# Performance work log

Hardware: AMD Instinct MI355X
Metric: run time of the kernel (lower is better)

Reference implementation:

```python
import jax, jax.numpy as jnp
import numpy as np

MODEL_DIM = 256
NUM_HEAD = 8
HEAD_DIM = MODEL_DIM // NUM_HEAD  # 32
ROT_DIM_AXIS = int(0.5 * HEAD_DIM)  # 16 per axis, 32 total rotated channels
LN_EPS = 1e-5
MASK_BIAS = -1e9  # fp32 precision
SCALE = HEAD_DIM ** -0.5
INIT_RANGE = 0.02
N_LAYERS = 6


def _rotate_half(x):
    # interleaved pairs: (d r) with r=2 -> (-x2, x1) re-interleaved
    x = x.reshape(*x.shape[:-1], -1, 2)
    x1, x2 = x[..., 0], x[..., 1]
    return jnp.stack([-x2, x1], axis=-1).reshape(*x.shape[:-2], -1)


def _axial_freqs(seqlen):
    # RotaryEmbedding('lang' freqs) over t = linspace(-1, 1, seqlen)
    inv_freq = 1.0 / (10000.0 ** (jnp.arange(0, ROT_DIM_AXIS, 2, dtype=jnp.float32) / ROT_DIM_AXIS))
    t = jnp.linspace(-1.0, 1.0, seqlen, dtype=jnp.float32)
    f = jnp.repeat(t[:, None] * inv_freq[None, :], 2, axis=-1)  # (s, ROT_DIM_AXIS)
    fh = jnp.broadcast_to(f[:, None, :], (seqlen, seqlen, ROT_DIM_AXIS))
    fw = jnp.broadcast_to(f[None, :, :], (seqlen, seqlen, ROT_DIM_AXIS))
    return jnp.concatenate([fh, fw], axis=-1)  # (s, s, 2*ROT_DIM_AXIS)


def _apply_rotary(freqs, t):
    rot_dim = freqs.shape[-1]
    t_rot, t_pass = t[..., :rot_dim], t[..., rot_dim:]
    t_rot = t_rot * jnp.cos(freqs) + _rotate_half(t_rot) * jnp.sin(freqs)
    return jnp.concatenate([t_rot, t_pass], axis=-1)


def setup_inputs() -> dict:
    key = jax.random.key(0)
    k1, k2, k3, k4 = jax.random.split(key, 4)
    b, s = 2, 128
    pair_act = jax.random.normal(k1, (b, s, s, MODEL_DIM), dtype=jnp.float32)
    pair_mask = jax.random.randint(k2, (b, s, s), 0, 2).astype(bool)  # True = masked
    Wqkv = jax.random.normal(k3, (3 * MODEL_DIM, MODEL_DIM), dtype=jnp.float32) * INIT_RANGE
    Wout = jax.random.normal(k4, (MODEL_DIM, MODEL_DIM), dtype=jnp.float32) * (INIT_RANGE / np.sqrt(2 * N_LAYERS))
    ln_gamma = jnp.ones((MODEL_DIM,), dtype=jnp.float32)
    ln_beta = jnp.zeros((MODEL_DIM,), dtype=jnp.float32)
    return {"pair_act": pair_act, "pair_mask": pair_mask, "ln_gamma": ln_gamma,
            "ln_beta": ln_beta, "Wqkv": Wqkv, "Wout": Wout}


def reference(pair_act, pair_mask, ln_gamma, ln_beta, Wqkv, Wout):
    # orientation == 'per_row': no axis swap
    b, s = pair_act.shape[0], pair_act.shape[1]
    # LayerNorm over model_dim
    mu = jnp.mean(pair_act, axis=-1, keepdims=True)
    var = jnp.var(pair_act, axis=-1, keepdims=True)
    x = (pair_act - mu) * jax.lax.rsqrt(var + LN_EPS) * ln_gamma + ln_beta
    # QKV projection (no bias)
    qkv = jnp.einsum('bxyd,ed->bxye', x, Wqkv)  # (b, s, s, 3*MODEL_DIM)
    q, k, v = jnp.split(qkv, 3, axis=-1)
    # 2D axial rotary on first 2*ROT_DIM_AXIS channels of the feature dim
    freqs = _axial_freqs(s)  # (s, s, 32)
    q = _apply_rotary(freqs, q)
    k = _apply_rotary(freqs, k)
    # multihead attention per row (axis s1 independent)
    q = q.reshape(b, s, s, NUM_HEAD, HEAD_DIM)
    k = k.reshape(b, s, s, NUM_HEAD, HEAD_DIM)
    v = v.reshape(b, s, s, NUM_HEAD, HEAD_DIM)
    scores = jnp.einsum('bxqhd,bxkhd->bxhqk', q, k) * SCALE  # (b, s1, h, s2, s2)
    mask = pair_mask[:, :, None, None, :]  # (b, s1, 1, 1, s2)
    scores = jnp.where(mask, MASK_BIAS, scores)
    attn = jax.nn.softmax(scores, axis=-1)
    out = jnp.einsum('bxhqk,bxkhd->bxqhd', attn, v).reshape(b, s, s, MODEL_DIM)
    return jnp.einsum('bxyd,ed->bxye', out, Wout)
```

## Files before the change

kernel.cpp:

```cpp
#include <hip/hip_runtime.h>
#include <math.h>
#include <stdint.h>

typedef __attribute__((ext_vector_type(8))) short short8;
typedef __attribute__((ext_vector_type(4))) float floatx4;

#define LN_EPS 1e-5f
#define ATT_SCALE 0.17677669529663687f

__device__ __constant__ float INVF[8] = {
    1.0f, 0.31622776601683794f, 0.1f, 0.031622776601683794f,
    0.01f, 0.0031622776601683794f, 0.001f, 0.00031622776601683794f};

__device__ inline unsigned short f2bf(float f) {
    unsigned u = __float_as_uint(f);
    u += 0x7fffu + ((u >> 16) & 1u);
    return (unsigned short)(u >> 16);
}

__device__ inline void gl_lds16(const unsigned short* g, unsigned short* l) {
    __builtin_amdgcn_global_load_lds(
        (const __attribute__((address_space(1))) void*)(uintptr_t)g,
        (__attribute__((address_space(3))) void*)(uintptr_t)l, 16, 0, 0);
}

__device__ inline void stage_tile(const unsigned short* __restrict__ Wsrc,
                                  unsigned short* dst, int w, int lane) {
    #pragma unroll
    for (int i = 0; i < 4; ++i) {
        int rbase = i * 16 + w * 2;
        int row = rbase + (lane >> 5);
        int sl = lane & 31;
        int c = (sl & ~7) | ((sl & 7) ^ (row & 7));
        gl_lds16(Wsrc + (size_t)row * 256 + c * 8, dst + rbase * 256);
    }
}

#define VM0() asm volatile("s_waitcnt vmcnt(0)" ::: "memory")
#define LG0() asm volatile("s_waitcnt lgkmcnt(0)" ::: "memory")
#define SBAR()                                 \
    do {                                       \
        __builtin_amdgcn_s_barrier();          \
        __builtin_amdgcn_sched_barrier(0);     \
    } while (0)

__global__ __launch_bounds__(256)
void prep_w(const float* __restrict__ wq, const float* __restrict__ wo,
            unsigned short* __restrict__ bq, unsigned short* __restrict__ bo) {
    int g = blockIdx.x * 256 + threadIdx.x;
    const float* src;
    unsigned short* dst;
    if (g < 49152) { src = wq + (size_t)g * 4; dst = bq + (size_t)g * 4; }
    else { int h = g - 49152; src = wo + (size_t)h * 4; dst = bo + (size_t)h * 4; }
    float4 v = *(const float4*)src;
    uint2 o;
    o.x = (unsigned)f2bf(v.x) | ((unsigned)f2bf(v.y) << 16);
    o.y = (unsigned)f2bf(v.z) | ((unsigned)f2bf(v.w) << 16);
    *(uint2*)dst = o;
}

__global__ __launch_bounds__(512, 2)
void fused_kernel(const float* __restrict__ pair_act, const int* __restrict__ mask,
                  const float* __restrict__ gamma, const float* __restrict__ beta,
                  const unsigned short* __restrict__ Wqkv,
                  const unsigned short* __restrict__ Wout,
                  float* __restrict__ out) {
    __shared__ __align__(16) unsigned short S16[2][16384];
    __shared__ __align__(16) unsigned short Ks[2][128 * 40];
    __shared__ __align__(16) unsigned short Vt[2][32 * 136];
    __shared__ __align__(16) unsigned short Qall[8 * 640];

    int bx = blockIdx.x;
    int tid = threadIdx.x;
    int w = tid >> 6, lane = tid & 63, qd = lane >> 4, lo = lane & 15;
    unsigned short* Qscr = Qall + w * 640;

    float tX = -1.0f + (2.0f / 127.0f) * (float)(bx & 127);

    stage_tile(Wqkv, &S16[1][0], w, lane);

    float msel[8];
    #pragma unroll
    for (int nt = 0; nt < 8; ++nt)
        msel[nt] = mask[bx * 128 + nt * 16 + lo] ? 0.0f : 1.0f;

    short8 a_frag[8];
    {
        int rl = tid >> 2, q0 = tid & 3;
        const float* src = pair_act + ((size_t)(bx * 128 + rl)) * 256 + q0 * 4;
        float4 v[16];
        float s = 0.f;
        #pragma unroll
        for (int u = 0; u < 16; ++u) {
            v[u] = *(const float4*)(src + u * 16);
            s += v[u].x + v[u].y + v[u].z + v[u].w;
        }
        s += __shfl_xor(s, 1);
        s += __shfl_xor(s, 2);
        float mean = s * (1.0f / 256.0f);
        float sq = 0.f;
        #pragma unroll
        for (int u = 0; u < 16; ++u) {
            float d0 = v[u].x - mean, d1 = v[u].y - mean;
            float d2 = v[u].z - mean, d3 = v[u].w - mean;
            sq += d0 * d0 + d1 * d1 + d2 * d2 + d3 * d3;
        }
        sq += __shfl_xor(sq, 1);
        sq += __shfl_xor(sq, 2);
        float rs = rsqrtf(sq * (1.0f / 256.0f) + LN_EPS);

        int rw = 16 * w + lo;
        #pragma unroll
        for (int p = 0; p < 2; ++p) {
            #pragma unroll
            for (int ul = 0; ul < 8; ++ul) {
                int u = p * 8 + ul;
                float4 g4 = *(const float4*)(gamma + q0 * 4 + u * 16);
                float4 b4 = *(const float4*)(beta + q0 * 4 + u * 16);
                unsigned e0 = f2bf((v[u].x - mean) * rs * g4.x + b4.x);
                unsigned e1 = f2bf((v[u].y - mean) * rs * g4.y + b4.y);
                unsigned e2 = f2bf((v[u].z - mean) * rs * g4.z + b4.z);
                unsigned e3 = f2bf((v[u].w - mean) * rs * g4.w + b4.w);
                int cw = 2 * ul + (q0 >> 1);
                int ss = (cw & ~7) | ((cw & 7) ^ (rl & 7));
                uint2 pk;
                pk.x = e0 | (e1 << 16);
                pk.y = e2 | (e3 << 16);
                *(uint2*)&S16[0][rl * 128 + ss * 8 + (q0 & 1) * 4] = pk;
            }
            __syncthreads();
            #pragma unroll
            for (int cp = 0; cp < 4; ++cp) {
                int ci = cp * 4 + qd;
                int ss = (ci & ~7) | ((ci & 7) ^ (rw & 7));
                a_frag[p * 4 + cp] = *(const short8*)&S16[0][rw * 128 + ss * 8];
            }
            __syncthreads();
        }
    }

    unsigned q_pk[4][4][2], k_pk[4][4][2], v_pk[4][4][2];
    #pragma unroll
    for (int t = 0; t < 12; ++t) {
        VM0();
        SBAR();
        const unsigned short* nsrc =
            (t < 11) ? (Wqkv + (size_t)(t + 1) * 64 * 256) : Wout;
        stage_tile(nsrc, &S16[t & 1][0], w, lane);

        const unsigned short* Sb = &S16[(t + 1) & 1][0];
        floatx4 acc[4];
        #pragma unroll
        for (int tq = 0; tq < 4; ++tq) acc[tq] = (floatx4){0.f, 0.f, 0.f, 0.f};
        #pragma unroll
        for (int cc = 0; cc < 8; ++cc) {
            #pragma unroll
            for (int tq = 0; tq < 4; ++tq) {
                int rw2 = tq * 16 + lo;
                int ci = cc * 4 + qd;
                int ss = (ci & ~7) | ((ci & 7) ^ (rw2 & 7));
                short8 bf = *(const short8*)&Sb[rw2 * 256 + ss * 8];
                acc[tq] = __builtin_amdgcn_mfma_f32_16x16x32_bf16(
                    a_frag[cc], bf, acc[tq], 0, 0, 0);
            }
        }
        if (t == 0 || t == 4) {
            #pragma unroll
            for (int tc = 0; tc < 2; ++tc) {
                int pi = (tc * 16 + lo) >> 1;
                float invf = INVF[pi & 7];
                float sgn = (lo & 1) ? 1.0f : -1.0f;
                #pragma unroll
                for (int r = 0; r < 4; ++r) {
                    int y = 16 * w + qd * 4 + r;
                    float tp = (pi < 8) ? tX
                                        : (-1.0f + (2.0f / 127.0f) * (float)y);
                    float sn, cs;
                    __sincosf(tp * invf, &sn, &cs);
                    float vv = acc[tc][r];
                    float pv = __shfl_xor(vv, 1);
                    acc[tc][r] = vv * cs + sgn * pv * sn;
                }
            }
        }
        int part = t >> 2, hc = t & 3;
        #pragma unroll
        for (int tq = 0; tq < 4; ++tq) {
            unsigned p0 = (unsigned)f2bf(acc[tq][0]) |
                          ((unsigned)f2bf(acc[tq][1]) << 16);
            unsigned p1 = (unsigned)f2bf(acc[tq][2]) |
                          ((unsigned)f2bf(acc[tq][3]) << 16);
            if (part == 0) { q_pk[hc][tq][0] = p0; q_pk[hc][tq][1] = p1; }
            else if (part == 1) { k_pk[hc][tq][0] = p0; k_pk[hc][tq][1] = p1; }
            else { v_pk[hc][tq][0] = p0; v_pk[hc][tq][1] = p1; }
        }
    }

    {
        #pragma unroll
        for (int tt = 0; tt < 2; ++tt) {
            int tC = tt;
            int d = tt * 16 + lo;
            #pragma unroll
            for (int r = 0; r < 4; ++r) {
                unsigned kv = (k_pk[0][tC][r >> 1] >> ((r & 1) * 16)) & 0xffffu;
                Ks[0][(16 * w + qd * 4 + r) * 40 + d] = (unsigned short)kv;
            }
            uint2 pv;
            pv.x = v_pk[0][tC][0];
            pv.y = v_pk[0][tC][1];
            *(uint2*)&Vt[0][d * 136 + 16 * w + qd * 4] = pv;
        }
    }
    LG0();
    SBAR();
    stage_tile(Wout + (size_t)64 * 256, &S16[0][0], w, lane);

    short8 of[8];
    #pragma unroll
    for (int h = 0; h < 8; ++h) {
        if (h < 7) {
            int g = h + 1, hcg = g >> 1, tg0 = (g & 1) * 2, kb = g & 1;
            #pragma unroll
            for (int tt = 0; tt < 2; ++tt) {
                int tC = tg0 + tt;
                int d = tt * 16 + lo;
                #pragma unroll
                for (int r = 0; r < 4; ++r) {
                    unsigned kv =
                        (k_pk[hcg][tC][r >> 1] >> ((r & 1) * 16)) & 0xffffu;
                    Ks[kb][(16 * w + qd * 4 + r) * 40 + d] = (unsigned short)kv;
                }
                uint2 pv;
                pv.x = v_pk[hcg][tC][0];
                pv.y = v_pk[hcg][tC][1];
                *(uint2*)&Vt[kb][d * 136 + 16 * w + qd * 4] = pv;
            }
        }
        {
            int hch = h >> 1, cb = h & 1;
            #pragma unroll
            for (int tt = 0; tt < 2; ++tt) {
                int tC = (h & 1) * 2 + tt;
                #pragma unroll
                for (int r = 0; r < 4; ++r) {
                    unsigned qv =
                        (q_pk[hch][tC][r >> 1] >> ((r & 1) * 16)) & 0xffffu;
                    Qscr[(qd * 4 + r) * 40 + tt * 16 + lo] = (unsigned short)qv;
                }
            }
            short8 aq = *(const short8*)&Qscr[lo * 40 + qd * 8];
            float ef[8][4];
            float sums[4] = {0.f, 0.f, 0.f, 0.f};
            #pragma unroll
            for (int nt = 0; nt < 8; ++nt) {
                short8 bk = *(const short8*)&Ks[cb][(nt * 16 + lo) * 40 + qd * 8];
                floatx4 c = (floatx4){0.f, 0.f, 0.f, 0.f};
                c = __builtin_amdgcn_mfma_f32_16x16x32_bf16(aq, bk, c, 0, 0, 0);
                #pragma unroll
                for (int r = 0; r < 4; ++r) {
                    float e = __expf(c[r] * ATT_SCALE) * msel[nt];
                    ef[nt][r] = e;
                    sums[r] += e;
                }
            }
            float inv[4];
            #pragma unroll
            for (int r = 0; r < 4; ++r) {
                float vv = sums[r];
                vv += __shfl_xor(vv, 1);
                vv += __shfl_xor(vv, 2);
                vv += __shfl_xor(vv, 4);
                vv += __shfl_xor(vv, 8);
                inv[r] = 1.0f / vv;
            }
            floatx4 o2[2];
            o2[0] = (floatx4){0.f, 0.f, 0.f, 0.f};
            o2[1] = (floatx4){0.f, 0.f, 0.f, 0.f};
            #pragma unroll
            for (int c2 = 0; c2 < 4; ++c2) {
                #pragma unroll
                for (int half = 0; half < 2; ++half) {
                    int nt = c2 * 2 + half;
                    #pragma unroll
                    for (int r = 0; r < 4; ++r)
                        Qscr[(qd * 4 + r) * 40 + half * 16 + lo] =
                            f2bf(ef[nt][r]);
                }
                short8 pa = *(const short8*)&Qscr[lo * 40 + qd * 8];
                #pragma unroll
                for (int n = 0; n < 2; ++n) {
                    short8 vb = *(const short8*)&Vt[cb][(n * 16 + lo) * 136 +
                                                       c2 * 32 + qd * 8];
                    o2[n] = __builtin_amdgcn_mfma_f32_16x16x32_bf16(pa, vb,
                                                                    o2[n], 0, 0, 0);
                }
            }
            #pragma unroll
            for (int n = 0; n < 2; ++n)
                #pragma unroll
                for (int r = 0; r < 4; ++r)
                    Qscr[(qd * 4 + r) * 40 + n * 16 + lo] =
                        f2bf(o2[n][r] * inv[r]);
            of[h] = *(const short8*)&Qscr[lo * 40 + qd * 8];
        }
        LG0();
        if (h == 7) VM0();
        SBAR();
    }

    #pragma unroll
    for (int nc = 0; nc < 4; ++nc) {
        if (nc) {
            VM0();
            SBAR();
            if (nc < 3)
                stage_tile(Wout + (size_t)(nc + 1) * 64 * 256,
                           &S16[nc & 1][0], w, lane);
        }
        const unsigned short* Sb = &S16[(nc + 1) & 1][0];
        floatx4 acc[4];
        #pragma unroll
        for (int tq = 0; tq < 4; ++tq) acc[tq] = (floatx4){0.f, 0.f, 0.f, 0.f};
        #pragma unroll
        for (int cc = 0; cc < 8; ++cc) {
            #pragma unroll
            for (int tq = 0; tq < 4; ++tq) {
                int rw2 = tq * 16 + lo;
                int ci = cc * 4 + qd;
                int ss = (ci & ~7) | ((ci & 7) ^ (rw2 & 7));
                short8 bf = *(const short8*)&Sb[rw2 * 256 + ss * 8];
                acc[tq] = __builtin_amdgcn_mfma_f32_16x16x32_bf16(
                    of[cc], bf, acc[tq], 0, 0, 0);
            }
        }
        #pragma unroll
        for (int tq = 0; tq < 4; ++tq)
            #pragma unroll
            for (int r = 0; r < 4; ++r)
                out[(size_t)(bx * 128 + 16 * w + qd * 4 + r) * 256 + nc * 64 +
                    tq * 16 + lo] = acc[tq][r];
    }
}

extern "C" void kernel_launch(void* const* d_in, const int* in_sizes, int n_in,
                              void* d_out, int out_size, void* d_ws, size_t ws_size,
                              hipStream_t stream) {
    const float* pair_act = (const float*)d_in[0];
    const int* pair_mask = (const int*)d_in[1];
    const float* ln_gamma = (const float*)d_in[2];
    const float* ln_beta = (const float*)d_in[3];
    const float* Wqkv = (const float*)d_in[4];
    const float* Wout = (const float*)d_in[5];
    float* out = (float*)d_out;

    char* ws = (char*)d_ws;
    unsigned short* wqkv_bf = (unsigned short*)ws;
    unsigned short* wout_bf = (unsigned short*)(ws + 393216);

    prep_w<<<256, 256, 0, stream>>>(Wqkv, Wout, wqkv_bf, wout_bf);
    fused_kernel<<<256, 512, 0, stream>>>(pair_act, pair_mask, ln_gamma, ln_beta,
                                          wqkv_bf, wout_bf, out);
}
```

Before: 138.3 us.

## Compute transposed scores and route P to MFMA A-operand via lane shuffles

The attention inner loop now computes S^T (K as A operand, Q as B) so each lane holds scores per key, then packs exp values to bf16 and redistributes them with ds_bpermute shuffles into the A-operand layout for the PV MFMA, instead of staging P through LDS scratch. Score, exp and PV MMA are interleaved per 32-key chunk, and the row sum is reduced with two shuffles. The Q fragment for the next head is prefetched into a double-buffered scratch region, doubling per-wave Q scratch LDS. This removes LDS round trips and register pressure from holding all exp values, at the cost of many cross-lane shuffles and extra mask broadcasts.

```diff
diff --git a/kernel.cpp b/kernel.cpp
--- a/kernel.cpp
+++ b/kernel.cpp
@@ -68,12 +68,12 @@
     __shared__ __align__(16) unsigned short S16[2][16384];
     __shared__ __align__(16) unsigned short Ks[2][128 * 40];
     __shared__ __align__(16) unsigned short Vt[2][32 * 136];
-    __shared__ __align__(16) unsigned short Qall[8 * 640];
+    __shared__ __align__(16) unsigned short Qall[8 * 1280];
 
     int bx = blockIdx.x;
     int tid = threadIdx.x;
     int w = tid >> 6, lane = tid & 63, qd = lane >> 4, lo = lane & 15;
-    unsigned short* Qscr = Qall + w * 640;
+    unsigned short* Qscr = Qall + w * 1280;
 
     float tX = -1.0f + (2.0f / 127.0f) * (float)(bx & 127);
 
@@ -196,6 +196,13 @@
         }
     }
 
+    float m2[8][4];
+    #pragma unroll
+    for (int nt = 0; nt < 8; ++nt)
+        #pragma unroll
+        for (int r = 0; r < 4; ++r)
+            m2[nt][r] = __shfl(msel[nt], qd * 4 + r);
+
     {
         #pragma unroll
         for (int tt = 0; tt < 2; ++tt) {
@@ -216,6 +223,14 @@
     SBAR();
     stage_tile(Wout + (size_t)64 * 256, &S16[0][0], w, lane);
 
+    #pragma unroll
+    for (int tt = 0; tt < 2; ++tt)
+        #pragma unroll
+        for (int r = 0; r < 4; ++r) {
+            unsigned qv = (q_pk[0][tt][r >> 1] >> ((r & 1) * 16)) & 0xffffu;
+            Qscr[(qd * 4 + r) * 40 + tt * 16 + lo] = (unsigned short)qv;
+        }
+
     short8 of[8];
     #pragma unroll
     for (int h = 0; h < 8; ++h) {
@@ -238,71 +253,84 @@
             }
         }
         {
-            int hch = h >> 1, cb = h & 1;
-            #pragma unroll
-            for (int tt = 0; tt < 2; ++tt) {
-                int tC = (h & 1) * 2 + tt;
-                #pragma unroll
-                for (int r = 0; r < 4; ++r) {
-                    unsigned qv =
-                        (q_pk[hch][tC][r >> 1] >> ((r & 1) * 16)) & 0xffffu;
-                    Qscr[(qd * 4 + r) * 40 + tt * 16 + lo] = (unsigned short)qv;
-                }
-            }
-            short8 aq = *(const short8*)&Qscr[lo * 40 + qd * 8];
-            float ef[8][4];
-            float sums[4] = {0.f, 0.f, 0.f, 0.f};
-            #pragma unroll
-            for (int nt = 0; nt < 8; ++nt) {
-                short8 bk = *(const short8*)&Ks[cb][(nt * 16 + lo) * 40 + qd * 8];
-                floatx4 c = (floatx4){0.f, 0.f, 0.f, 0.f};
-                c = __builtin_amdgcn_mfma_f32_16x16x32_bf16(aq, bk, c, 0, 0, 0);
-                #pragma unroll
-                for (int r = 0; r < 4; ++r) {
-                    float e = __expf(c[r] * ATT_SCALE) * msel[nt];
-                    ef[nt][r] = e;
-                    sums[r] += e;
-                }
-            }
-            float inv[4];
-            #pragma unroll
-            for (int r = 0; r < 4; ++r) {
-                float vv = sums[r];
-                vv += __shfl_xor(vv, 1);
-                vv += __shfl_xor(vv, 2);
-                vv += __shfl_xor(vv, 4);
-                vv += __shfl_xor(vv, 8);
-                inv[r] = 1.0f / vv;
-            }
+            int cb = h & 1;
+            short8 aq = *(const short8*)&Qscr[(h & 1) * 640 + lo * 40 + qd * 8];
+            if (h < 7) {
+                int hn = h + 1, hch = hn >> 1;
+                #pragma unroll
+                for (int tt = 0; tt < 2; ++tt) {
+                    int tC = (hn & 1) * 2 + tt;
+                    #pragma unroll
+                    for (int r = 0; r < 4; ++r) {
+                        unsigned qv =
+                            (q_pk[hch][tC][r >> 1] >> ((r & 1) * 16)) & 0xffffu;
+                        Qscr[(hn & 1) * 640 + (qd * 4 + r) * 40 + tt * 16 + lo] =
+                            (unsigned short)qv;
+                    }
+                }
+            }
+            int idx1 = (qd & 1) * 32 + lo;
+            int idx2 = idx1 + 16;
+            int sel = qd >> 1;
+            float lsum = 0.f;
             floatx4 o2[2];
             o2[0] = (floatx4){0.f, 0.f, 0.f, 0.f};
             o2[1] = (floatx4){0.f, 0.f, 0.f, 0.f};
             #pragma unroll
             for (int c2 = 0; c2 < 4; ++c2) {
-                #pragma unroll
-                for (int half = 0; half < 2; ++half) {
-                    int nt = c2 * 2 + half;
-                    #pragma unroll
-                    for (int r = 0; r < 4; ++r)
-                        Qscr[(qd * 4 + r) * 40 + half * 16 + lo] =
-                            f2bf(ef[nt][r]);
-                }
-                short8 pa = *(const short8*)&Qscr[lo * 40 + qd * 8];
+                short8 bk0 =
+                    *(const short8*)&Ks[cb][((2 * c2) * 16 + lo) * 40 + qd * 8];
+                short8 bk1 =
+                    *(const short8*)&Ks[cb][((2 * c2 + 1) * 16 + lo) * 40 + qd * 8];
+                floatx4 s0 = (floatx4){0.f, 0.f, 0.f, 0.f};
+                floatx4 s1 = (floatx4){0.f, 0.f, 0.f, 0.f};
+                s0 = __builtin_amdgcn_mfma_f32_16x16x32_bf16(bk0, aq, s0, 0, 0, 0);
+                s1 = __builtin_amdgcn_mfma_f32_16x16x32_bf16(bk1, aq, s1, 0, 0, 0);
+                float eA[4], eB[4];
+                #pragma unroll
+                for (int r = 0; r < 4; ++r) {
+                    eA[r] = __expf(s0[r] * ATT_SCALE) * m2[2 * c2][r];
+                    eB[r] = __expf(s1[r] * ATT_SCALE) * m2[2 * c2 + 1][r];
+                    lsum += eA[r] + eB[r];
+                }
+                unsigned P0d0 = (unsigned)f2bf(eA[0]) | ((unsigned)f2bf(eA[1]) << 16);
+                unsigned P0d1 = (unsigned)f2bf(eA[2]) | ((unsigned)f2bf(eA[3]) << 16);
+                unsigned P1d0 = (unsigned)f2bf(eB[0]) | ((unsigned)f2bf(eB[1]) << 16);
+                unsigned P1d1 = (unsigned)f2bf(eB[2]) | ((unsigned)f2bf(eB[3]) << 16);
+                unsigned t10 = (unsigned)__shfl((int)P0d0, idx1);
+                unsigned t11 = (unsigned)__shfl((int)P0d1, idx1);
+                unsigned t12 = (unsigned)__shfl((int)P1d0, idx1);
+                unsigned t13 = (unsigned)__shfl((int)P1d1, idx1);
+                unsigned t20 = (unsigned)__shfl((int)P0d0, idx2);
+                unsigned t21 = (unsigned)__shfl((int)P0d1, idx2);
+                unsigned t22 = (unsigned)__shfl((int)P1d0, idx2);
+                unsigned t23 = (unsigned)__shfl((int)P1d1, idx2);
+                union { unsigned u[4]; short8 s8; } pa;
+                pa.u[0] = sel ? t12 : t10;
+                pa.u[1] = sel ? t13 : t11;
+                pa.u[2] = sel ? t22 : t20;
+                pa.u[3] = sel ? t23 : t21;
                 #pragma unroll
                 for (int n = 0; n < 2; ++n) {
                     short8 vb = *(const short8*)&Vt[cb][(n * 16 + lo) * 136 +
-                                                       c2 * 32 + qd * 8];
-                    o2[n] = __builtin_amdgcn_mfma_f32_16x16x32_bf16(pa, vb,
+                                                        c2 * 32 + qd * 8];
+                    o2[n] = __builtin_amdgcn_mfma_f32_16x16x32_bf16(pa.s8, vb,
                                                                     o2[n], 0, 0, 0);
                 }
             }
+            lsum += __shfl_xor(lsum, 16);
+            lsum += __shfl_xor(lsum, 32);
+            float invs = 1.0f / lsum;
+            float inv_q[4];
+            #pragma unroll
+            for (int r = 0; r < 4; ++r) inv_q[r] = __shfl(invs, qd * 4 + r);
             #pragma unroll
             for (int n = 0; n < 2; ++n)
                 #pragma unroll
                 for (int r = 0; r < 4; ++r)
-                    Qscr[(qd * 4 + r) * 40 + n * 16 + lo] =
-                        f2bf(o2[n][r] * inv[r]);
-            of[h] = *(const short8*)&Qscr[lo * 40 + qd * 8];
+                    Qscr[(h & 1) * 640 + (qd * 4 + r) * 40 + n * 16 + lo] =
+                        f2bf(o2[n][r] * inv_q[r]);
+            of[h] = *(const short8*)&Qscr[(h & 1) * 640 + lo * 40 + qd * 8];
         }
         LG0();
         if (h == 7) VM0();
```

Measured after the change: 140.2 us. No clear change (+1.4%).
